# Optimization experiments

Measured on AMD Instinct MI355X. Metric: run time of the kernel, lower is better.

## Reference

```python
import jax, jax.numpy as jnp
import numpy as np

B, H, S, D = 2, 16, 2048, 64

def setup_inputs() -> dict:
    key = jax.random.key(0)
    kq, kk, kv = jax.random.split(key, 3)
    query = jax.random.normal(kq, (B, H, S, D), dtype=jnp.float32)
    k_ = jax.random.normal(kk, (B, H, S, D), dtype=jnp.float32)
    value = jax.random.normal(kv, (B, H, S, D), dtype=jnp.float32)
    # causal bool mask: True = masked (matches torch masked_fill semantics)
    attn_mask = jnp.triu(jnp.ones((S, S), dtype=bool), k=1)
    # no padding (all False) so no softmax row is fully masked
    key_padding_mask = jnp.zeros((B, S), dtype=bool)
    return {"query": query, "key": k_, "value": value,
            "attn_mask": attn_mask, "key_padding_mask": key_padding_mask}

def reference(query, key, value, attn_mask, key_padding_mask):
    scale = query.shape[-1] ** -0.5
    # [B,H,Sq,Sk] scores
    scores = jnp.einsum('bhqd,bhkd->bhqk', query, key) * scale
    scores = jnp.where(key_padding_mask[:, None, None, :], -jnp.inf, scores)
    scores = jnp.where(attn_mask, -jnp.inf, scores)
    attn = jax.nn.softmax(scores, axis=-1)
    # dropout=0.0 -> identity in eval/math
    return jnp.einsum('bhqk,bhkd->bhqd', attn, value)
```

## Files before the change

### kernel.cpp

```cpp
#include <hip/hip_runtime.h>
#include <hip/hip_bf16.h>


#define BHN 32
#define SEQ 2048
#define DIM 64
#define NW  4
#define LSTR 72

typedef __attribute__((ext_vector_type(8))) short  short8;
typedef __attribute__((ext_vector_type(4))) short  short4v;
typedef __attribute__((ext_vector_type(4))) float  float4v;

__device__ __forceinline__ short f2b(float x) {
  __hip_bfloat16 h = __float2bfloat16(x);
  return __builtin_bit_cast(short, h);
}

__global__ __launch_bounds__(256) void prep_kernel(
    const float* __restrict__ K, const float* __restrict__ V,
    __hip_bfloat16* __restrict__ Kb, __hip_bfloat16* __restrict__ Vt) {
  __shared__ float t[64][65];
  const int bh = blockIdx.x, j = blockIdx.y, tid = threadIdx.x;
  const int r = tid >> 2, seg = (tid & 3) * 16;
  const size_t base = (size_t)bh * SEQ * DIM;
  {
    const float* ks = K + base + (size_t)(j * 64 + r) * DIM + seg;
    float4v k0 = *(const float4v*)(ks + 0);
    float4v k1 = *(const float4v*)(ks + 4);
    float4v k2 = *(const float4v*)(ks + 8);
    float4v k3 = *(const float4v*)(ks + 12);
    short8 a, b;
    a[0]=f2b(k0[0]); a[1]=f2b(k0[1]); a[2]=f2b(k0[2]); a[3]=f2b(k0[3]);
    a[4]=f2b(k1[0]); a[5]=f2b(k1[1]); a[6]=f2b(k1[2]); a[7]=f2b(k1[3]);
    b[0]=f2b(k2[0]); b[1]=f2b(k2[1]); b[2]=f2b(k2[2]); b[3]=f2b(k2[3]);
    b[4]=f2b(k3[0]); b[5]=f2b(k3[1]); b[6]=f2b(k3[2]); b[7]=f2b(k3[3]);
    __hip_bfloat16* kd = Kb + base + (size_t)(j * 64 + r) * DIM + seg;
    *(short8*)kd = a;
    *(short8*)(kd + 8) = b;
  }
  {
    const float* src = V + base + (size_t)(j * 64 + r) * DIM + seg;
    float4v f0 = *(const float4v*)(src + 0);
    float4v f1 = *(const float4v*)(src + 4);
    float4v f2 = *(const float4v*)(src + 8);
    float4v f3 = *(const float4v*)(src + 12);
    *(float4v*)&t[r][seg + 0]  = f0;
    *(float4v*)&t[r][seg + 4]  = f1;
    *(float4v*)&t[r][seg + 8]  = f2;
    *(float4v*)&t[r][seg + 12] = f3;
    __syncthreads();
    short8 o0, o1;
    #pragma unroll
    for (int i = 0; i < 8; ++i) o0[i] = f2b(t[seg + i][r]);
    #pragma unroll
    for (int i = 0; i < 8; ++i) o1[i] = f2b(t[seg + 8 + i][r]);
    __hip_bfloat16* dst = Vt + (size_t)bh * DIM * SEQ + (size_t)r * SEQ + j * 64 + seg;
    *(short8*)dst = o0;
    *(short8*)(dst + 8) = o1;
  }
}

__global__ __launch_bounds__(256) void fattn4(
    const float* __restrict__ Qg, const __hip_bfloat16* __restrict__ Kb,
    const __hip_bfloat16* __restrict__ Vt, float* __restrict__ Og) {
  __shared__ alignas(16) __hip_bfloat16 kt[64][LSTR];
  __shared__ alignas(16) __hip_bfloat16 vt[64][LSTR];
  __shared__ alignas(16) __hip_bfloat16 pt[NW][16][LSTR];

  const int bh   = blockIdx.x;
  const int qt   = gridDim.y - 1 - blockIdx.y;
  const int tid  = threadIdx.x;
  const int wave = tid >> 6;
  const int lane = tid & 63;
  const int ln   = lane & 15;
  const int quad = lane >> 4;
  const size_t base  = (size_t)bh * SEQ * DIM;
  const size_t baseV = (size_t)bh * DIM * SEQ;
  const int q0 = qt * 64;

  const float QSCALE = 0.125f * 1.44269504088896340736f;
  short8 qf[2];
  {
    const int qrow = q0 + wave * 16 + ln;
    const float* qp = Qg + base + (size_t)qrow * DIM + quad * 8;
    #pragma unroll
    for (int kk = 0; kk < 2; ++kk) {
      float4v f0 = *(const float4v*)(qp + kk * 32);
      float4v f1 = *(const float4v*)(qp + kk * 32 + 4);
      short8 qv;
      qv[0] = f2b(f0[0] * QSCALE); qv[1] = f2b(f0[1] * QSCALE);
      qv[2] = f2b(f0[2] * QSCALE); qv[3] = f2b(f0[3] * QSCALE);
      qv[4] = f2b(f1[0] * QSCALE); qv[5] = f2b(f1[1] * QSCALE);
      qv[6] = f2b(f1[2] * QSCALE); qv[7] = f2b(f1[3] * QSCALE);
      qf[kk] = qv;
    }
  }

  float4v o[4];
  #pragma unroll
  for (int dt = 0; dt < 4; ++dt) { float4v z = {0.f,0.f,0.f,0.f}; o[dt] = z; }
  float4v accl = {0.f, 0.f, 0.f, 0.f};

  short8 ones;
  #pragma unroll
  for (int x = 0; x < 8; ++x) ones[x] = (short)0x3F80;

  const int srow = tid >> 2;
  const int scol = (tid & 3) * 16;

  short8 ka0, ka1, va0, va1;
  {
    const __hip_bfloat16* kp = Kb + base + (size_t)srow * DIM + scol;
    ka0 = *(const short8*)kp; ka1 = *(const short8*)(kp + 8);
    const __hip_bfloat16* vp = Vt + baseV + (size_t)srow * SEQ + scol;
    va0 = *(const short8*)vp; va1 = *(const short8*)(vp + 8);
  }

  for (int j = 0; j <= qt; ++j) {
    *(short8*)&kt[srow][scol]     = ka0;
    *(short8*)&kt[srow][scol + 8] = ka1;
    *(short8*)&vt[srow][scol]     = va0;
    *(short8*)&vt[srow][scol + 8] = va1;
    __syncthreads();

    if (j < qt) {
      const int kb = (j + 1) * 64;
      const __hip_bfloat16* kp = Kb + base + (size_t)(kb + srow) * DIM + scol;
      ka0 = *(const short8*)kp; ka1 = *(const short8*)(kp + 8);
      const __hip_bfloat16* vp = Vt + baseV + (size_t)srow * SEQ + kb + scol;
      va0 = *(const short8*)vp; va1 = *(const short8*)(vp + 8);
    }

    float4v s[4];
    #pragma unroll
    for (int nt = 0; nt < 4; ++nt) {
      short8 b0 = *(const short8*)&kt[nt * 16 + ln][quad * 8];
      short8 b1 = *(const short8*)&kt[nt * 16 + ln][32 + quad * 8];
      float4v acc = {0.f,0.f,0.f,0.f};
      acc = __builtin_amdgcn_mfma_f32_16x16x32_bf16(qf[0], b0, acc, 0, 0, 0);
      acc = __builtin_amdgcn_mfma_f32_16x16x32_bf16(qf[1], b1, acc, 0, 0, 0);
      s[nt] = acc;
    }

    if (j == qt) {
      #pragma unroll
      for (int nt = 0; nt < 4; ++nt) {
        const int col = nt * 16 + ln;
        #pragma unroll
        for (int rg = 0; rg < 4; ++rg)
          if (col > wave * 16 + quad * 4 + rg) s[nt][rg] = -1e30f;
      }
    }

    #pragma unroll
    for (int nt = 0; nt < 4; ++nt)
      #pragma unroll
      for (int rg = 0; rg < 4; ++rg)
        pt[wave][quad * 4 + rg][nt * 16 + ln] =
            __float2bfloat16(__builtin_amdgcn_exp2f(s[nt][rg]));

    short8 pa0 = *(const short8*)&pt[wave][ln][quad * 8];
    short8 pa1 = *(const short8*)&pt[wave][ln][32 + quad * 8];

    accl = __builtin_amdgcn_mfma_f32_16x16x32_bf16(pa0, ones, accl, 0, 0, 0);
    accl = __builtin_amdgcn_mfma_f32_16x16x32_bf16(pa1, ones, accl, 0, 0, 0);

    #pragma unroll
    for (int dt = 0; dt < 4; ++dt) {
      short8 vb0 = *(const short8*)&vt[dt * 16 + ln][quad * 8];
      short8 vb1 = *(const short8*)&vt[dt * 16 + ln][32 + quad * 8];
      o[dt] = __builtin_amdgcn_mfma_f32_16x16x32_bf16(pa0, vb0, o[dt], 0, 0, 0);
      o[dt] = __builtin_amdgcn_mfma_f32_16x16x32_bf16(pa1, vb1, o[dt], 0, 0, 0);
    }
    __syncthreads();
  }

  #pragma unroll
  for (int rg = 0; rg < 4; ++rg) {
    const float inv = 1.0f / accl[rg];
    const int row = q0 + wave * 16 + quad * 4 + rg;
    float* op = Og + base + (size_t)row * DIM + ln;
    #pragma unroll
    for (int dt = 0; dt < 4; ++dt)
      op[dt * 16] = o[dt][rg] * inv;
  }
}

__global__ __launch_bounds__(256) void fattn_ref(
    const float* __restrict__ Qg, const float* __restrict__ Kg,
    const float* __restrict__ Vg, float* __restrict__ Og) {
  __shared__ alignas(16) __hip_bfloat16 kt[64][LSTR];
  __shared__ alignas(16) __hip_bfloat16 vt[64][LSTR];
  __shared__ alignas(16) __hip_bfloat16 pt[NW][16][LSTR];

  const int bh   = blockIdx.x;
  const int qt   = gridDim.y - 1 - blockIdx.y;
  const int tid  = threadIdx.x;
  const int wave = tid >> 6;
  const int lane = tid & 63;
  const int ln   = lane & 15;
  const int quad = lane >> 4;
  const size_t base = (size_t)bh * SEQ * DIM;
  const int q0 = qt * 64;

  const float QSCALE = 0.125f * 1.44269504088896340736f;
  short8 qf[2];
  {
    const int qrow = q0 + wave * 16 + ln;
    const float* qp = Qg + base + (size_t)qrow * DIM + quad * 8;
    #pragma unroll
    for (int kk = 0; kk < 2; ++kk) {
      float4v f0 = *(const float4v*)(qp + kk * 32);
      float4v f1 = *(const float4v*)(qp + kk * 32 + 4);
      short8 qv;
      qv[0] = f2b(f0[0] * QSCALE); qv[1] = f2b(f0[1] * QSCALE);
      qv[2] = f2b(f0[2] * QSCALE); qv[3] = f2b(f0[3] * QSCALE);
      qv[4] = f2b(f1[0] * QSCALE); qv[5] = f2b(f1[1] * QSCALE);
      qv[6] = f2b(f1[2] * QSCALE); qv[7] = f2b(f1[3] * QSCALE);
      qf[kk] = qv;
    }
  }
  float4v o[4];
  #pragma unroll
  for (int dt = 0; dt < 4; ++dt) { float4v z = {0.f,0.f,0.f,0.f}; o[dt] = z; }
  float l_i[4] = {0.f, 0.f, 0.f, 0.f};

  for (int j = 0; j <= qt; ++j) {
    const int kbase = j * 64;
    __syncthreads();
    {
      const int r = tid >> 4, c = (tid & 15) * 4;
      #pragma unroll
      for (int it = 0; it < 4; ++it) {
        const int row = it * 16 + r;
        float4v f = *(const float4v*)(Kg + base + (size_t)(kbase + row) * DIM + c);
        short4v sv; sv[0]=f2b(f[0]); sv[1]=f2b(f[1]); sv[2]=f2b(f[2]); sv[3]=f2b(f[3]);
        *(short4v*)&kt[row][c] = sv;
      }
      const int d = tid & 63, s0 = (tid >> 6) * 4;
      #pragma unroll
      for (int it = 0; it < 4; ++it) {
        const int sk = it * 16 + s0;
        short4v sv;
        sv[0] = f2b(Vg[base + (size_t)(kbase + sk + 0) * DIM + d]);
        sv[1] = f2b(Vg[base + (size_t)(kbase + sk + 1) * DIM + d]);
        sv[2] = f2b(Vg[base + (size_t)(kbase + sk + 2) * DIM + d]);
        sv[3] = f2b(Vg[base + (size_t)(kbase + sk + 3) * DIM + d]);
        *(short4v*)&vt[d][sk] = sv;
      }
    }
    __syncthreads();

    float4v s[4];
    #pragma unroll
    for (int nt = 0; nt < 4; ++nt) {
      short8 b0 = *(const short8*)&kt[nt * 16 + ln][quad * 8];
      short8 b1 = *(const short8*)&kt[nt * 16 + ln][32 + quad * 8];
      float4v acc = {0.f,0.f,0.f,0.f};
      acc = __builtin_amdgcn_mfma_f32_16x16x32_bf16(qf[0], b0, acc, 0, 0, 0);
      acc = __builtin_amdgcn_mfma_f32_16x16x32_bf16(qf[1], b1, acc, 0, 0, 0);
      s[nt] = acc;
    }
    if (j == qt) {
      #pragma unroll
      for (int nt = 0; nt < 4; ++nt) {
        const int col = nt * 16 + ln;
        #pragma unroll
        for (int rg = 0; rg < 4; ++rg)
          if (col > wave * 16 + quad * 4 + rg) s[nt][rg] = -1e30f;
      }
    }
    #pragma unroll
    for (int rg = 0; rg < 4; ++rg) {
      float p0 = __builtin_amdgcn_exp2f(s[0][rg]);
      float p1 = __builtin_amdgcn_exp2f(s[1][rg]);
      float p2 = __builtin_amdgcn_exp2f(s[2][rg]);
      float p3 = __builtin_amdgcn_exp2f(s[3][rg]);
      s[0][rg]=p0; s[1][rg]=p1; s[2][rg]=p2; s[3][rg]=p3;
      float rs = (p0 + p1) + (p2 + p3);
      rs += __shfl_xor(rs, 1, 64); rs += __shfl_xor(rs, 2, 64);
      rs += __shfl_xor(rs, 4, 64); rs += __shfl_xor(rs, 8, 64);
      l_i[rg] += rs;
    }
    #pragma unroll
    for (int nt = 0; nt < 4; ++nt)
      #pragma unroll
      for (int rg = 0; rg < 4; ++rg)
        pt[wave][quad * 4 + rg][nt * 16 + ln] = __float2bfloat16(s[nt][rg]);
    short8 pa0 = *(const short8*)&pt[wave][ln][quad * 8];
    short8 pa1 = *(const short8*)&pt[wave][ln][32 + quad * 8];
    #pragma unroll
    for (int dt = 0; dt < 4; ++dt) {
      short8 vb0 = *(const short8*)&vt[dt * 16 + ln][quad * 8];
      short8 vb1 = *(const short8*)&vt[dt * 16 + ln][32 + quad * 8];
      o[dt] = __builtin_amdgcn_mfma_f32_16x16x32_bf16(pa0, vb0, o[dt], 0, 0, 0);
      o[dt] = __builtin_amdgcn_mfma_f32_16x16x32_bf16(pa1, vb1, o[dt], 0, 0, 0);
    }
  }
  #pragma unroll
  for (int rg = 0; rg < 4; ++rg) {
    const float inv = 1.0f / l_i[rg];
    const int row = q0 + wave * 16 + quad * 4 + rg;
    float* op = Og + base + (size_t)row * DIM + ln;
    #pragma unroll
    for (int dt = 0; dt < 4; ++dt) op[dt * 16] = o[dt][rg] * inv;
  }
}

extern "C" void kernel_launch(void* const* d_in, const int* in_sizes, int n_in,
                              void* d_out, int out_size, void* d_ws, size_t ws_size,
                              hipStream_t stream) {
  (void)in_sizes; (void)n_in; (void)out_size;
  const float* Q = (const float*)d_in[0];
  const float* K = (const float*)d_in[1];
  const float* V = (const float*)d_in[2];
  float* O = (float*)d_out;
  const size_t need = (size_t)2 * BHN * SEQ * DIM * sizeof(__hip_bfloat16);
  if (ws_size >= need) {
    __hip_bfloat16* Kb = (__hip_bfloat16*)d_ws;
    __hip_bfloat16* Vt = Kb + (size_t)BHN * SEQ * DIM;
    prep_kernel<<<dim3(BHN, SEQ / 64), 256, 0, stream>>>(K, V, Kb, Vt);
    fattn4<<<dim3(BHN, SEQ / 64), 256, 0, stream>>>(Q, Kb, Vt, O);
  } else {
    fattn_ref<<<dim3(BHN, SEQ / 64), 256, 0, stream>>>(Q, K, V, O);
  }
}
```

Measured before the change: 147.9 us.

## Rewrite attention kernel with 32x32 MFMA, 128-row query tiles and double-buffered KV

Replaces the 16x16x32 MFMA attention kernel with one using 32x32x16 MFMA. Each wave now owns 32 query rows, so a block covers 128 rows and the grid is halved. K/V tiles are double-buffered in LDS so the prefetch store overlaps compute, and one barrier per iteration is removed. The probabilities stay in registers and are packed with v_cvt_pk_bf16 and lane shuffles instead of a round-trip through LDS, and row sums are accumulated in-register rather than via an MFMA against ones. This trades fewer blocks and more registers per thread (launch bound of 2 blocks per SM) for more reuse of each K/V tile and less LDS traffic.

New measurement: 147.7 us. About the same (-0.2%).

```diff
diff --git a/kernel.cpp b/kernel.cpp
--- a/kernel.cpp
+++ b/kernel.cpp
@@ -8,9 +8,11 @@
 #define NW  4
 #define LSTR 72
 
-typedef __attribute__((ext_vector_type(8))) short  short8;
-typedef __attribute__((ext_vector_type(4))) short  short4v;
-typedef __attribute__((ext_vector_type(4))) float  float4v;
+typedef __attribute__((ext_vector_type(8)))  short    short8;
+typedef __attribute__((ext_vector_type(4)))  short    short4v;
+typedef __attribute__((ext_vector_type(4)))  float    float4v;
+typedef __attribute__((ext_vector_type(16))) float    f32x16;
+typedef __attribute__((ext_vector_type(4)))  unsigned uint4v;
 
 __device__ __forceinline__ short f2b(float x) {
   __hip_bfloat16 h = __float2bfloat16(x);
@@ -61,50 +63,47 @@
   }
 }
 
-__global__ __launch_bounds__(256) void fattn4(
+__global__ __launch_bounds__(256, 2) void fattn6(
     const float* __restrict__ Qg, const __hip_bfloat16* __restrict__ Kb,
     const __hip_bfloat16* __restrict__ Vt, float* __restrict__ Og) {
-  __shared__ alignas(16) __hip_bfloat16 kt[64][LSTR];
-  __shared__ alignas(16) __hip_bfloat16 vt[64][LSTR];
-  __shared__ alignas(16) __hip_bfloat16 pt[NW][16][LSTR];
+  __shared__ alignas(16) __hip_bfloat16 kt[2][64][LSTR];
+  __shared__ alignas(16) __hip_bfloat16 vt[2][64][LSTR];
+  __shared__ float lbuf[NW][32];
 
   const int bh   = blockIdx.x;
   const int qt   = gridDim.y - 1 - blockIdx.y;
   const int tid  = threadIdx.x;
-  const int wave = tid >> 6;
+  const int w    = tid >> 6;
   const int lane = tid & 63;
-  const int ln   = lane & 15;
-  const int quad = lane >> 4;
+  const int l31  = lane & 31;
+  const int hi   = lane >> 5;
   const size_t base  = (size_t)bh * SEQ * DIM;
   const size_t baseV = (size_t)bh * DIM * SEQ;
-  const int q0 = qt * 64;
+  const int q0   = qt * 128;
+  const int jmax = 2 * qt + 1;
 
   const float QSCALE = 0.125f * 1.44269504088896340736f;
-  short8 qf[2];
-  {
-    const int qrow = q0 + wave * 16 + ln;
-    const float* qp = Qg + base + (size_t)qrow * DIM + quad * 8;
-    #pragma unroll
-    for (int kk = 0; kk < 2; ++kk) {
-      float4v f0 = *(const float4v*)(qp + kk * 32);
-      float4v f1 = *(const float4v*)(qp + kk * 32 + 4);
+
+  short8 qf[4];
+  {
+    const float* qp = Qg + base + (size_t)(q0 + 32 * w + l31) * DIM + 8 * hi;
+    #pragma unroll
+    for (int s = 0; s < 4; ++s) {
+      float4v f0 = *(const float4v*)(qp + 16 * s);
+      float4v f1 = *(const float4v*)(qp + 16 * s + 4);
       short8 qv;
       qv[0] = f2b(f0[0] * QSCALE); qv[1] = f2b(f0[1] * QSCALE);
       qv[2] = f2b(f0[2] * QSCALE); qv[3] = f2b(f0[3] * QSCALE);
       qv[4] = f2b(f1[0] * QSCALE); qv[5] = f2b(f1[1] * QSCALE);
       qv[6] = f2b(f1[2] * QSCALE); qv[7] = f2b(f1[3] * QSCALE);
-      qf[kk] = qv;
-    }
-  }
-
-  float4v o[4];
+      qf[s] = qv;
+    }
+  }
+
+  f32x16 o0, o1;
   #pragma unroll
-  for (int dt = 0; dt < 4; ++dt) { float4v z = {0.f,0.f,0.f,0.f}; o[dt] = z; }
-  float4v accl = {0.f, 0.f, 0.f, 0.f};
-
-  short8 ones;
-  #pragma unroll
-  for (int x = 0; x < 8; ++x) ones[x] = (short)0x3F80;
+  for (int i = 0; i < 16; ++i) { o0[i] = 0.f; o1[i] = 0.f; }
+  float acc_l = 0.f;
 
   const int srow = tid >> 2;
   const int scol = (tid & 3) * 16;
@@ -116,15 +115,16 @@
     const __hip_bfloat16* vp = Vt + baseV + (size_t)srow * SEQ + scol;
     va0 = *(const short8*)vp; va1 = *(const short8*)(vp + 8);
   }
-
-  for (int j = 0; j <= qt; ++j) {
-    *(short8*)&kt[srow][scol]     = ka0;
-    *(short8*)&kt[srow][scol + 8] = ka1;
-    *(short8*)&vt[srow][scol]     = va0;
-    *(short8*)&vt[srow][scol + 8] = va1;
-    __syncthreads();
-
-    if (j < qt) {
+  *(short8*)&kt[0][srow][scol]     = ka0;
+  *(short8*)&kt[0][srow][scol + 8] = ka1;
+  *(short8*)&vt[0][srow][scol]     = va0;
+  *(short8*)&vt[0][srow][scol + 8] = va1;
+  __syncthreads();
+
+  for (int j = 0; j <= jmax; ++j) {
+    const int cur = j & 1;
+
+    if (j < jmax) {
       const int kb = (j + 1) * 64;
       const __hip_bfloat16* kp = Kb + base + (size_t)(kb + srow) * DIM + scol;
       ka0 = *(const short8*)kp; ka1 = *(const short8*)(kp + 8);
@@ -132,58 +132,100 @@
       va0 = *(const short8*)vp; va1 = *(const short8*)(vp + 8);
     }
 
-    float4v s[4];
-    #pragma unroll
-    for (int nt = 0; nt < 4; ++nt) {
-      short8 b0 = *(const short8*)&kt[nt * 16 + ln][quad * 8];
-      short8 b1 = *(const short8*)&kt[nt * 16 + ln][32 + quad * 8];
-      float4v acc = {0.f,0.f,0.f,0.f};
-      acc = __builtin_amdgcn_mfma_f32_16x16x32_bf16(qf[0], b0, acc, 0, 0, 0);
-      acc = __builtin_amdgcn_mfma_f32_16x16x32_bf16(qf[1], b1, acc, 0, 0, 0);
-      s[nt] = acc;
-    }
-
-    if (j == qt) {
-      #pragma unroll
-      for (int nt = 0; nt < 4; ++nt) {
-        const int col = nt * 16 + ln;
+    const bool act = (64 * j <= q0 + 32 * w + 31);
+    unsigned pw[16];
+
+    if (act) {
+      f32x16 p0, p1;
+      #pragma unroll
+      for (int i = 0; i < 16; ++i) { p0[i] = 0.f; p1[i] = 0.f; }
+      __builtin_amdgcn_s_setprio(1);
+      #pragma unroll
+      for (int s = 0; s < 4; ++s) {
+        short8 a0 = *(const short8*)&kt[cur][l31][16 * s + 8 * hi];
+        short8 a1 = *(const short8*)&kt[cur][32 + l31][16 * s + 8 * hi];
+        p0 = __builtin_amdgcn_mfma_f32_32x32x16_bf16(a0, qf[s], p0, 0, 0, 0);
+        p1 = __builtin_amdgcn_mfma_f32_32x32x16_bf16(a1, qf[s], p1, 0, 0, 0);
+      }
+      __builtin_amdgcn_s_setprio(0);
+
+      if (64 * j + 63 > q0 + 32 * w) {
+        const int qg  = q0 + 32 * w + l31;
+        const int kb0 = 64 * j + 4 * hi;
         #pragma unroll
-        for (int rg = 0; rg < 4; ++rg)
-          if (col > wave * 16 + quad * 4 + rg) s[nt][rg] = -1e30f;
-      }
-    }
-
-    #pragma unroll
-    for (int nt = 0; nt < 4; ++nt)
-      #pragma unroll
-      for (int rg = 0; rg < 4; ++rg)
-        pt[wave][quad * 4 + rg][nt * 16 + ln] =
-            __float2bfloat16(__builtin_amdgcn_exp2f(s[nt][rg]));
-
-    short8 pa0 = *(const short8*)&pt[wave][ln][quad * 8];
-    short8 pa1 = *(const short8*)&pt[wave][ln][32 + quad * 8];
-
-    accl = __builtin_amdgcn_mfma_f32_16x16x32_bf16(pa0, ones, accl, 0, 0, 0);
-    accl = __builtin_amdgcn_mfma_f32_16x16x32_bf16(pa1, ones, accl, 0, 0, 0);
-
-    #pragma unroll
-    for (int dt = 0; dt < 4; ++dt) {
-      short8 vb0 = *(const short8*)&vt[dt * 16 + ln][quad * 8];
-      short8 vb1 = *(const short8*)&vt[dt * 16 + ln][32 + quad * 8];
-      o[dt] = __builtin_amdgcn_mfma_f32_16x16x32_bf16(pa0, vb0, o[dt], 0, 0, 0);
-      o[dt] = __builtin_amdgcn_mfma_f32_16x16x32_bf16(pa1, vb1, o[dt], 0, 0, 0);
+        for (int r = 0; r < 16; ++r) {
+          const int kr = kb0 + (r & 3) + 8 * (r >> 2);
+          if (kr > qg)      p0[r] = -1e30f;
+          if (kr + 32 > qg) p1[r] = -1e30f;
+        }
+      }
+
+      #pragma unroll
+      for (int i = 0; i < 16; ++i) {
+        p0[i] = __builtin_amdgcn_exp2f(p0[i]);
+        p1[i] = __builtin_amdgcn_exp2f(p1[i]);
+      }
+      #pragma unroll
+      for (int i = 0; i < 8; ++i)
+        asm("v_cvt_pk_bf16_f32 %0, %1, %2"
+            : "=v"(pw[i]) : "v"(p0[2 * i]), "v"(p0[2 * i + 1]));
+      #pragma unroll
+      for (int i = 0; i < 8; ++i)
+        asm("v_cvt_pk_bf16_f32 %0, %1, %2"
+            : "=v"(pw[8 + i]) : "v"(p1[2 * i]), "v"(p1[2 * i + 1]));
+
+      float rs = 0.f;
+      #pragma unroll
+      for (int i = 0; i < 16; ++i) {
+        rs += __builtin_bit_cast(float, pw[i] << 16);
+        rs += __builtin_bit_cast(float, pw[i] & 0xffff0000u);
+      }
+      rs += __shfl_xor(rs, 32, 64);
+      acc_l += rs;
+    }
+
+    if (j < jmax) {
+      const int nb = cur ^ 1;
+      *(short8*)&kt[nb][srow][scol]     = ka0;
+      *(short8*)&kt[nb][srow][scol + 8] = ka1;
+      *(short8*)&vt[nb][srow][scol]     = va0;
+      *(short8*)&vt[nb][srow][scol + 8] = va1;
+    }
+
+    if (act) {
+      #pragma unroll
+      for (int t = 0; t < 4; ++t) {
+        const unsigned x0 = __shfl_xor(pw[4 * t + 0], 32, 64);
+        const unsigned x1 = __shfl_xor(pw[4 * t + 1], 32, 64);
+        const unsigned x2 = __shfl_xor(pw[4 * t + 2], 32, 64);
+        const unsigned x3 = __shfl_xor(pw[4 * t + 3], 32, 64);
+        const unsigned f0 = hi ? x2 : pw[4 * t + 0];
+        const unsigned f1 = hi ? x3 : pw[4 * t + 1];
+        const unsigned f2 = hi ? pw[4 * t + 2] : x0;
+        const unsigned f3 = hi ? pw[4 * t + 3] : x1;
+        uint4v u = {f0, f1, f2, f3};
+        short8 pa = __builtin_bit_cast(short8, u);
+        short8 b0 = *(const short8*)&vt[cur][l31][16 * t + 8 * hi];
+        short8 b1 = *(const short8*)&vt[cur][32 + l31][16 * t + 8 * hi];
+        __builtin_amdgcn_s_setprio(1);
+        o0 = __builtin_amdgcn_mfma_f32_32x32x16_bf16(pa, b0, o0, 0, 0, 0);
+        o1 = __builtin_amdgcn_mfma_f32_32x32x16_bf16(pa, b1, o1, 0, 0, 0);
+        __builtin_amdgcn_s_setprio(0);
+      }
     }
     __syncthreads();
   }
 
+  if (lane < 32) lbuf[w][l31] = acc_l;
+  __syncthreads();
+  const float* lb = lbuf[w];
+  float* op = Og + base + (size_t)(q0 + 32 * w) * DIM + l31;
   #pragma unroll
-  for (int rg = 0; rg < 4; ++rg) {
-    const float inv = 1.0f / accl[rg];
-    const int row = q0 + wave * 16 + quad * 4 + rg;
-    float* op = Og + base + (size_t)row * DIM + ln;
-    #pragma unroll
-    for (int dt = 0; dt < 4; ++dt)
-      op[dt * 16] = o[dt][rg] * inv;
+  for (int r = 0; r < 16; ++r) {
+    const int row = (r & 3) + 8 * (r >> 2) + 4 * hi;
+    const float iv = 1.0f / lb[row];
+    op[(size_t)row * DIM]      = o0[r] * iv;
+    op[(size_t)row * DIM + 32] = o1[r] * iv;
   }
 }
 
@@ -321,7 +363,7 @@
     __hip_bfloat16* Kb = (__hip_bfloat16*)d_ws;
     __hip_bfloat16* Vt = Kb + (size_t)BHN * SEQ * DIM;
     prep_kernel<<<dim3(BHN, SEQ / 64), 256, 0, stream>>>(K, V, Kb, Vt);
-    fattn4<<<dim3(BHN, SEQ / 64), 256, 0, stream>>>(Q, Kb, Vt, O);
+    fattn6<<<dim3(BHN, SEQ / 128), 256, 0, stream>>>(Q, Kb, Vt, O);
   } else {
     fattn_ref<<<dim3(BHN, SEQ / 64), 256, 0, stream>>>(Q, K, V, O);
   }
```
